# Kernel tuning notes

Measured on AMD Instinct MI355X. Metric: run time of the kernel, lower is better.

The kernel has to match this reference:

```python
import jax, jax.numpy as jnp
import numpy as np

EMBED = 128
NUM_HOPS = 3
VOCAB = 32000
MEM = 50
PAD = 0


def pos_weights(J, d):
    # MemN2N position encoding: 1 - (j+1)/J - (k+1)/d * (1 - 2*(j+1)/J)
    j = jnp.arange(J, dtype=jnp.float32)[:, None]
    k = jnp.arange(d, dtype=jnp.float32)[None, :]
    return 1.0 - (j + 1.0) / J - (k + 1.0) / d * (1.0 - 2.0 * (j + 1.0) / J)


def setup_inputs() -> dict:
    key = jax.random.key(0)
    ks = jax.random.split(key, 10)
    ctx_query = jax.random.randint(ks[0], (16, 10, 20), 0, VOCAB)
    story = jax.random.randint(ks[1], (16, MEM, 40), 0, VOCAB)

    def emb(k):
        w = 0.1 * jax.random.normal(k, (VOCAB, EMBED), dtype=jnp.float32)
        return w.at[PAD].set(0.0)  # padding_idx row is zero

    A_w = emb(ks[2])
    C_w = emb(ks[3])
    B_w = emb(ks[4])
    H_w = 0.1 * jax.random.normal(ks[5], (EMBED, EMBED), dtype=jnp.float32)
    H_b = 0.1 * jax.random.normal(ks[6], (EMBED,), dtype=jnp.float32)
    out_w = 0.1 * jax.random.normal(ks[7], (VOCAB, EMBED), dtype=jnp.float32)
    TA = 0.1 * jax.random.normal(ks[8], (MEM, EMBED), dtype=jnp.float32)
    TC = 0.1 * jax.random.normal(ks[9], (MEM, EMBED), dtype=jnp.float32)
    return {"ctx_query": ctx_query, "story": story, "A_w": A_w, "C_w": C_w,
            "B_w": B_w, "H_w": H_w, "H_b": H_b, "out_w": out_w, "TA": TA, "TC": TC}


def reference(ctx_query, story, A_w, C_w, B_w, H_w, H_b, out_w, TA, TC):
    B, NQ, S = ctx_query.shape
    R, S2 = story.shape[1], story.shape[2]
    cq = ctx_query.reshape(B * NQ, S)
    # story repeated across num_qa (broadcast instead of materialized repeat)
    st = jnp.broadcast_to(story[:, None], (B, NQ, R, S2)).reshape(B * NQ, R, S2)

    qw = pos_weights(S, EMBED)            # [S, d]
    state = jnp.sum(B_w[cq] * qw, axis=1)  # [BN, d]

    sw = pos_weights(S2, EMBED)           # [S2, d]
    for _ in range(NUM_HOPS):             # use_lw=True: A/C tied across hops
        mem = jnp.sum(A_w[st] * sw, axis=2) + TA    # [BN, R, d]
        outm = jnp.sum(C_w[st] * sw, axis=2) + TC   # [BN, R, d]
        probs = jax.nn.softmax(jnp.einsum('brd,bd->br', mem, state), axis=-1)
        response = jnp.einsum('br,brd->bd', probs, outm)  # [BN, d]
        state = response @ H_w.T + H_b + state      # H(response) + state
    return state @ out_w.T                          # [BN, vocab]
```

## Files before the change

kernel.cpp:

```cpp
#include <hip/hip_runtime.h>
#include <hip/hip_bf16.h>
#include <math.h>

#define EMBED 128
#define VOCAB 32000
#define MEMN  50
#define BATCH 16
#define NQ    10
#define SQ    20
#define SS    40
#define BN    (BATCH*NQ)
#define NHOPS 3

typedef short v8s __attribute__((ext_vector_type(8)));
typedef float v4f __attribute__((ext_vector_type(4)));

__device__ __forceinline__ float posw(int j, int J, int k) {
    float jf = (float)(j + 1) / (float)J;
    return 1.0f - jf - ((float)(k + 1) / (float)EMBED) * (1.0f - 2.0f * jf);
}

__device__ __forceinline__ short f2bf(float f) {
    __hip_bfloat16 h = __float2bfloat16(f);
    return *(short*)&h;
}

__global__ void k_embed(const int* __restrict__ cq, const int* __restrict__ story,
                        const float* __restrict__ Bw, const float* __restrict__ Aw,
                        const float* __restrict__ Cw, const float* __restrict__ TA,
                        const float* __restrict__ TC, const float* __restrict__ Hw,
                        float* __restrict__ state, float* __restrict__ memb,
                        float* __restrict__ outb, float* __restrict__ HwT) {
    int blk = blockIdx.x;
    int t = threadIdx.x;
    if (blk < BN) {
        float acc = 0.f;
        #pragma unroll
        for (int s = 0; s < SQ; ++s) {
            int tok = cq[blk * SQ + s];
            acc += Bw[tok * EMBED + t] * posw(s, SQ, t);
        }
        state[blk * EMBED + t] = acc;
    } else if (blk < BN + BATCH * MEMN) {
        int br = blk - BN;
        int r = br % MEMN;
        float ma = TA[r * EMBED + t];
        float mc = TC[r * EMBED + t];
        const int* toks = story + br * SS;
        #pragma unroll 4
        for (int s = 0; s < SS; ++s) {
            int tok = toks[s];
            float w = posw(s, SS, t);
            ma += Aw[tok * EMBED + t] * w;
            mc += Cw[tok * EMBED + t] * w;
        }
        memb[br * EMBED + t] = ma;
        outb[br * EMBED + t] = mc;
    } else {
        int k = blk - (BN + BATCH * MEMN);
        HwT[k * EMBED + t] = Hw[t * EMBED + k];
    }
}

__global__ void k_hops(const float* __restrict__ memb, const float* __restrict__ outb,
                       const float* __restrict__ HwT, const float* __restrict__ Hb,
                       const float* __restrict__ state, __hip_bfloat16* __restrict__ stateF) {
    __shared__ float lmem[MEMN][EMBED + 1];
    __shared__ float lout[MEMN][EMBED + 1];
    __shared__ float lstate[EMBED];
    __shared__ float lprobs[MEMN];
    __shared__ float lresp[EMBED];
    int bn = blockIdx.x;
    int b  = bn / NQ;
    int t  = threadIdx.x;
    for (int i = t; i < MEMN * EMBED; i += EMBED) {
        int r = i >> 7, d = i & 127;
        lmem[r][d] = memb[b * MEMN * EMBED + i];
        lout[r][d] = outb[b * MEMN * EMBED + i];
    }
    lstate[t] = state[bn * EMBED + t];
    __syncthreads();

    for (int hop = 0; hop < NHOPS; ++hop) {
        float logit = -1e30f;
        if (t < MEMN) {
            float acc = 0.f;
            for (int d = 0; d < EMBED; ++d) acc += lmem[t][d] * lstate[d];
            logit = acc;
        }
        if (t < 64) {
            float m = logit;
            #pragma unroll
            for (int off = 32; off; off >>= 1) m = fmaxf(m, __shfl_xor(m, off, 64));
            float e = (t < MEMN) ? __expf(logit - m) : 0.f;
            float ssum = e;
            #pragma unroll
            for (int off = 32; off; off >>= 1) ssum += __shfl_xor(ssum, off, 64);
            if (t < MEMN) lprobs[t] = e / ssum;
        }
        __syncthreads();
        float resp = 0.f;
        for (int r = 0; r < MEMN; ++r) resp += lprobs[r] * lout[r][t];
        lresp[t] = resp;
        __syncthreads();
        float acc = Hb[t] + lstate[t];
        for (int k = 0; k < EMBED; ++k) acc += lresp[k] * HwT[k * EMBED + t];
        __syncthreads();
        lstate[t] = acc;
        __syncthreads();
    }
    int frag = ((t >> 5) << 2) | ((t >> 3) & 3);
    stateF[((size_t)frag * BN + bn) * 8 + (t & 7)] = __float2bfloat16(lstate[t]);
}

__global__ __launch_bounds__(64) void k_out(const __hip_bfloat16* __restrict__ stateF,
                                            const float* __restrict__ outw,
                                            float* __restrict__ out) {
    int l = threadIdx.x;
    int col16 = l & 15;
    int kg = l >> 4;
    int vbase = blockIdx.x << 4;
    int v = vbase + col16;

    v8s bfrag[4];
    #pragma unroll
    for (int k4 = 0; k4 < 4; ++k4) {
        const float4* p = (const float4*)&outw[(size_t)v * EMBED + k4 * 32 + kg * 8];
        float4 w0 = p[0], w1 = p[1];
        v8s bf;
        bf[0] = f2bf(w0.x); bf[1] = f2bf(w0.y); bf[2] = f2bf(w0.z); bf[3] = f2bf(w0.w);
        bf[4] = f2bf(w1.x); bf[5] = f2bf(w1.y); bf[6] = f2bf(w1.z); bf[7] = f2bf(w1.w);
        bfrag[k4] = bf;
    }

    v4f acc[10];
    #pragma unroll
    for (int m = 0; m < 10; ++m) acc[m] = (v4f){0.f, 0.f, 0.f, 0.f};

    const v8s* aF = (const v8s*)stateF;
    #pragma unroll
    for (int k4 = 0; k4 < 4; ++k4) {
        v8s af[10];
        #pragma unroll
        for (int m = 0; m < 10; ++m)
            af[m] = aF[(((k4 << 2) | kg) * BN) + m * 16 + col16];
        #pragma unroll
        for (int m = 0; m < 10; ++m)
            acc[m] = __builtin_amdgcn_mfma_f32_16x16x32_bf16(af[m], bfrag[k4], acc[m], 0, 0, 0);
    }

    #pragma unroll
    for (int m = 0; m < 10; ++m) {
        #pragma unroll
        for (int i = 0; i < 4; ++i)
            out[(size_t)(m * 16 + kg * 4 + i) * VOCAB + v] = acc[m][i];
    }
}

extern "C" void kernel_launch(void* const* d_in, const int* in_sizes, int n_in,
                              void* d_out, int out_size, void* d_ws, size_t ws_size,
                              hipStream_t stream) {
    const int*   ctx_query = (const int*)  d_in[0];
    const int*   story     = (const int*)  d_in[1];
    const float* A_w       = (const float*)d_in[2];
    const float* C_w       = (const float*)d_in[3];
    const float* B_w       = (const float*)d_in[4];
    const float* H_w       = (const float*)d_in[5];
    const float* H_b       = (const float*)d_in[6];
    const float* out_w     = (const float*)d_in[7];
    const float* TA        = (const float*)d_in[8];
    const float* TC        = (const float*)d_in[9];
    float* out = (float*)d_out;

    float* ws    = (float*)d_ws;
    float* state = ws;
    float* memb  = state + BN * EMBED;
    float* outb  = memb + BATCH * MEMN * EMBED;
    float* HwT   = outb + BATCH * MEMN * EMBED;
    __hip_bfloat16* stateF = (__hip_bfloat16*)(HwT + EMBED * EMBED);

    k_embed<<<BN + BATCH * MEMN + EMBED, EMBED, 0, stream>>>(
        ctx_query, story, B_w, A_w, C_w, TA, TC, H_w, state, memb, outb, HwT);
    k_hops<<<BN, EMBED, 0, stream>>>(memb, outb, HwT, H_b, state, stateF);
    k_out<<<VOCAB / 16, 64, 0, stream>>>(stateF, out_w, out);
}
```

Measured before the change: 36.78 us.

## Pre-convert output weights to bf16 in embed kernel and split A/C gathers

The fp32-to-bf16 conversion of out_w moves out of the output GEMM kernel and into extra blocks of the embedding kernel. There it runs alongside the gathers, and k_out then reads half the bytes. The A and C story gathers are split into separate blocks to raise parallelism, with full unrolling. The cost is an extra full write and read of an 8 MB bf16 copy of out_w in the workspace. The out_w read still happens once, just earlier, so the gain depends on overlap with the latency-bound embed work.

New measurement: 35.87 us. -2.5%, faster.

```diff
diff --git a/kernel.cpp b/kernel.cpp
--- a/kernel.cpp
+++ b/kernel.cpp
@@ -12,6 +12,13 @@
 #define BN    (BATCH*NQ)
 #define NHOPS 3
 
+#define G_QRY   BN
+#define G_STA   (G_QRY + BATCH*MEMN)
+#define G_STC   (G_STA + BATCH*MEMN)
+#define G_HT    (G_STC + EMBED)
+#define CONVROWS 64
+#define G_CONV  (G_HT + VOCAB/CONVROWS)
+
 typedef short v8s __attribute__((ext_vector_type(8)));
 typedef float v4f __attribute__((ext_vector_type(4)));
 
@@ -29,36 +36,56 @@
                         const float* __restrict__ Bw, const float* __restrict__ Aw,
                         const float* __restrict__ Cw, const float* __restrict__ TA,
                         const float* __restrict__ TC, const float* __restrict__ Hw,
+                        const float* __restrict__ outw,
                         float* __restrict__ state, float* __restrict__ memb,
-                        float* __restrict__ outb, float* __restrict__ HwT) {
+                        float* __restrict__ outb, float* __restrict__ HwT,
+                        __hip_bfloat16* __restrict__ owb) {
     int blk = blockIdx.x;
     int t = threadIdx.x;
-    if (blk < BN) {
+    if (blk < G_QRY) {
         float acc = 0.f;
+        const int* toks = cq + blk * SQ;
         #pragma unroll
         for (int s = 0; s < SQ; ++s) {
-            int tok = cq[blk * SQ + s];
+            int tok = toks[s];
             acc += Bw[tok * EMBED + t] * posw(s, SQ, t);
         }
         state[blk * EMBED + t] = acc;
-    } else if (blk < BN + BATCH * MEMN) {
-        int br = blk - BN;
+    } else if (blk < G_STA) {
+        int br = blk - G_QRY;
         int r = br % MEMN;
         float ma = TA[r * EMBED + t];
+        const int* toks = story + br * SS;
+        #pragma unroll
+        for (int s = 0; s < SS; ++s) {
+            int tok = toks[s];
+            ma += Aw[tok * EMBED + t] * posw(s, SS, t);
+        }
+        memb[br * EMBED + t] = ma;
+    } else if (blk < G_STC) {
+        int br = blk - G_STA;
+        int r = br % MEMN;
         float mc = TC[r * EMBED + t];
         const int* toks = story + br * SS;
-        #pragma unroll 4
+        #pragma unroll
         for (int s = 0; s < SS; ++s) {
             int tok = toks[s];
-            float w = posw(s, SS, t);
-            ma += Aw[tok * EMBED + t] * w;
-            mc += Cw[tok * EMBED + t] * w;
-        }
-        memb[br * EMBED + t] = ma;
+            mc += Cw[tok * EMBED + t] * posw(s, SS, t);
+        }
         outb[br * EMBED + t] = mc;
+    } else if (blk < G_HT) {
+        int k = blk - G_STC;
+        HwT[k * EMBED + t] = Hw[t * EMBED + k];
     } else {
-        int k = blk - (BN + BATCH * MEMN);
-        HwT[k * EMBED + t] = Hw[t * EMBED + k];
+        int base = (blk - G_HT) * (CONVROWS * EMBED);
+        #pragma unroll
+        for (int i = 0; i < 16; ++i) {
+            int e = base + i * 512 + t * 4;
+            float4 w = *(const float4*)&outw[e];
+            short4 p;
+            p.x = f2bf(w.x); p.y = f2bf(w.y); p.z = f2bf(w.z); p.w = f2bf(w.w);
+            *(short4*)&owb[e] = p;
+        }
     }
 }
 
@@ -73,10 +100,11 @@
     int bn = blockIdx.x;
     int b  = bn / NQ;
     int t  = threadIdx.x;
-    for (int i = t; i < MEMN * EMBED; i += EMBED) {
-        int r = i >> 7, d = i & 127;
-        lmem[r][d] = memb[b * MEMN * EMBED + i];
-        lout[r][d] = outb[b * MEMN * EMBED + i];
+    #pragma unroll
+    for (int i = 0; i < MEMN; ++i) {
+        int e = i * EMBED + t;
+        lmem[i][t] = memb[b * MEMN * EMBED + e];
+        lout[i][t] = outb[b * MEMN * EMBED + e];
     }
     lstate[t] = state[bn * EMBED + t];
     __syncthreads();
@@ -114,7 +142,7 @@
 }
 
 __global__ __launch_bounds__(64) void k_out(const __hip_bfloat16* __restrict__ stateF,
-                                            const float* __restrict__ outw,
+                                            const __hip_bfloat16* __restrict__ owb,
                                             float* __restrict__ out) {
     int l = threadIdx.x;
     int col16 = l & 15;
@@ -122,16 +150,11 @@
     int vbase = blockIdx.x << 4;
     int v = vbase + col16;
 
+    const v8s* bp = (const v8s*)owb;
     v8s bfrag[4];
     #pragma unroll
-    for (int k4 = 0; k4 < 4; ++k4) {
-        const float4* p = (const float4*)&outw[(size_t)v * EMBED + k4 * 32 + kg * 8];
-        float4 w0 = p[0], w1 = p[1];
-        v8s bf;
-        bf[0] = f2bf(w0.x); bf[1] = f2bf(w0.y); bf[2] = f2bf(w0.z); bf[3] = f2bf(w0.w);
-        bf[4] = f2bf(w1.x); bf[5] = f2bf(w1.y); bf[6] = f2bf(w1.z); bf[7] = f2bf(w1.w);
-        bfrag[k4] = bf;
-    }
+    for (int k4 = 0; k4 < 4; ++k4)
+        bfrag[k4] = bp[(size_t)v * 16 + k4 * 4 + kg];
 
     v4f acc[10];
     #pragma unroll
@@ -178,9 +201,11 @@
     float* outb  = memb + BATCH * MEMN * EMBED;
     float* HwT   = outb + BATCH * MEMN * EMBED;
     __hip_bfloat16* stateF = (__hip_bfloat16*)(HwT + EMBED * EMBED);
-
-    k_embed<<<BN + BATCH * MEMN + EMBED, EMBED, 0, stream>>>(
-        ctx_query, story, B_w, A_w, C_w, TA, TC, H_w, state, memb, outb, HwT);
-    k_hops<<<BN, EMBED, 0, stream>>>(memb, outb, HwT, H_b, state, stateF);
-    k_out<<<VOCAB / 16, 64, 0, stream>>>(stateF, out_w, out);
-}
+    __hip_bfloat16* owb    = stateF + BN * EMBED;
+
+    k_embed<<<G_CONV, 128, 0, stream>>>(
+        ctx_query, story, B_w, A_w, C_w, TA, TC, H_w, out_w,
+        state, memb, outb, HwT, owb);
+    k_hops<<<BN, 128, 0, stream>>>(memb, outb, HwT, H_b, state, stateF);
+    k_out<<<VOCAB / 16, 64, 0, stream>>>(stateF, owb, out);
+}
```

## Fuse hops and output GEMM into one kernel with atomic-counter handoff

Applied to the files above, without the earlier changes.

Merges the hop kernel and the vocabulary projection into a single launch. 160 blocks run the hops while 250 GEMM blocks prefetch and convert their out_w tiles to bf16, then spin on a global counter until every hop block has published its state. The hop blocks now use 256 threads with split reductions and read H_w directly, which drops the transpose work from the embed kernel. This removes one launch and overlaps weight loading with the serial hop chain. The cost is a spin-wait that assumes all 410 blocks can be resident at once, plus a smaller number of GEMM blocks each handling two tiles.

After: 124.6 us. +238.7%, slower.

```diff
diff --git a/kernel.cpp b/kernel.cpp
--- a/kernel.cpp
+++ b/kernel.cpp
@@ -12,8 +12,14 @@
 #define BN    (BATCH*NQ)
 #define NHOPS 3
 
+#define NHOPSBLK 160
+#define NGEMMBLK 250
+#define K2BLOCKS (NHOPSBLK + NGEMMBLK)
+
 typedef short v8s __attribute__((ext_vector_type(8)));
 typedef float v4f __attribute__((ext_vector_type(4)));
+
+#define MFMA16 __builtin_amdgcn_mfma_f32_16x16x32_bf16
 
 __device__ __forceinline__ float posw(int j, int J, int k) {
     float jf = (float)(j + 1) / (float)J;
@@ -28,9 +34,9 @@
 __global__ void k_embed(const int* __restrict__ cq, const int* __restrict__ story,
                         const float* __restrict__ Bw, const float* __restrict__ Aw,
                         const float* __restrict__ Cw, const float* __restrict__ TA,
-                        const float* __restrict__ TC, const float* __restrict__ Hw,
+                        const float* __restrict__ TC,
                         float* __restrict__ state, float* __restrict__ memb,
-                        float* __restrict__ outb, float* __restrict__ HwT) {
+                        float* __restrict__ outb, unsigned* __restrict__ counter) {
     int blk = blockIdx.x;
     int t = threadIdx.x;
     if (blk < BN) {
@@ -57,103 +63,165 @@
         memb[br * EMBED + t] = ma;
         outb[br * EMBED + t] = mc;
     } else {
-        int k = blk - (BN + BATCH * MEMN);
-        HwT[k * EMBED + t] = Hw[t * EMBED + k];
+        if (t == 0) *counter = 0u;
     }
 }
 
-__global__ void k_hops(const float* __restrict__ memb, const float* __restrict__ outb,
-                       const float* __restrict__ HwT, const float* __restrict__ Hb,
-                       const float* __restrict__ state, __hip_bfloat16* __restrict__ stateF) {
+__global__ __launch_bounds__(256) void k_fused(const float* __restrict__ memb,
+                                               const float* __restrict__ outb,
+                                               const float* __restrict__ Hw,
+                                               const float* __restrict__ Hb,
+                                               const float* __restrict__ state,
+                                               const float* __restrict__ outw,
+                                               __hip_bfloat16* __restrict__ stateF,
+                                               unsigned* __restrict__ counter,
+                                               float* __restrict__ out) {
     __shared__ float lmem[MEMN][EMBED + 1];
     __shared__ float lout[MEMN][EMBED + 1];
     __shared__ float lstate[EMBED];
-    __shared__ float lprobs[MEMN];
-    __shared__ float lresp[EMBED];
-    int bn = blockIdx.x;
-    int b  = bn / NQ;
-    int t  = threadIdx.x;
-    for (int i = t; i < MEMN * EMBED; i += EMBED) {
-        int r = i >> 7, d = i & 127;
-        lmem[r][d] = memb[b * MEMN * EMBED + i];
-        lout[r][d] = outb[b * MEMN * EMBED + i];
-    }
-    lstate[t] = state[bn * EMBED + t];
-    __syncthreads();
-
-    for (int hop = 0; hop < NHOPS; ++hop) {
-        float logit = -1e30f;
-        if (t < MEMN) {
-            float acc = 0.f;
-            for (int d = 0; d < EMBED; ++d) acc += lmem[t][d] * lstate[d];
-            logit = acc;
-        }
-        if (t < 64) {
-            float m = logit;
-            #pragma unroll
-            for (int off = 32; off; off >>= 1) m = fmaxf(m, __shfl_xor(m, off, 64));
-            float e = (t < MEMN) ? __expf(logit - m) : 0.f;
-            float ssum = e;
-            #pragma unroll
-            for (int off = 32; off; off >>= 1) ssum += __shfl_xor(ssum, off, 64);
-            if (t < MEMN) lprobs[t] = e / ssum;
-        }
+    __shared__ float lpart[4][52];
+    __shared__ float lprobs[52];
+    __shared__ float lrespp[2][EMBED];
+    __shared__ float lHp[2][EMBED];
+
+    int blk = blockIdx.x;
+    int t = threadIdx.x;
+    int w = t >> 6;
+    int l = t & 63;
+
+    if (blk < NHOPSBLK) {
+        int bn = blk;
+        int b  = bn / NQ;
+        int d  = t & 127;
+        int h  = t >> 7;
+
+        {
+            const float4* mb4 = (const float4*)(memb + (size_t)b * MEMN * EMBED);
+            const float4* ob4 = (const float4*)(outb + (size_t)b * MEMN * EMBED);
+            for (int i = t; i < MEMN * EMBED / 4; i += 256) {
+                int r = i >> 5, c = (i & 31) << 2;
+                float4 v = mb4[i];
+                lmem[r][c] = v.x; lmem[r][c+1] = v.y; lmem[r][c+2] = v.z; lmem[r][c+3] = v.w;
+                float4 u = ob4[i];
+                lout[r][c] = u.x; lout[r][c+1] = u.y; lout[r][c+2] = u.z; lout[r][c+3] = u.w;
+            }
+            if (t < EMBED) lstate[t] = state[bn * EMBED + t];
+        }
+        float hbd = (t < EMBED) ? Hb[t] : 0.f;
         __syncthreads();
-        float resp = 0.f;
-        for (int r = 0; r < MEMN; ++r) resp += lprobs[r] * lout[r][t];
-        lresp[t] = resp;
+
+        for (int hop = 0; hop < NHOPS; ++hop) {
+            if (l < MEMN) {
+                int d0 = w << 5;
+                float a0 = 0.f, a1 = 0.f, a2 = 0.f, a3 = 0.f;
+                #pragma unroll
+                for (int j = 0; j < 32; j += 4) {
+                    a0 += lmem[l][d0 + j]     * lstate[d0 + j];
+                    a1 += lmem[l][d0 + j + 1] * lstate[d0 + j + 1];
+                    a2 += lmem[l][d0 + j + 2] * lstate[d0 + j + 2];
+                    a3 += lmem[l][d0 + j + 3] * lstate[d0 + j + 3];
+                }
+                lpart[w][l] = (a0 + a1) + (a2 + a3);
+            }
+            __syncthreads();
+            if (t < 64) {
+                float lg = (t < MEMN)
+                    ? (lpart[0][t] + lpart[1][t]) + (lpart[2][t] + lpart[3][t]) : -1e30f;
+                float mx = lg;
+                #pragma unroll
+                for (int off = 32; off; off >>= 1) mx = fmaxf(mx, __shfl_xor(mx, off, 64));
+                float e = (t < MEMN) ? __expf(lg - mx) : 0.f;
+                float ss = e;
+                #pragma unroll
+                for (int off = 32; off; off >>= 1) ss += __shfl_xor(ss, off, 64);
+                if (t < MEMN) lprobs[t] = e / ss;
+            }
+            __syncthreads();
+            {
+                float r0 = 0.f, r1 = 0.f;
+                int k0 = h * 25;
+                #pragma unroll
+                for (int k = 0; k < 24; k += 2) {
+                    r0 += lprobs[k0 + k]     * lout[k0 + k][d];
+                    r1 += lprobs[k0 + k + 1] * lout[k0 + k + 1][d];
+                }
+                r0 += lprobs[k0 + 24] * lout[k0 + 24][d];
+                lrespp[h][d] = r0 + r1;
+            }
+            __syncthreads();
+            {
+                int ks = h << 6;
+                const float4* hw4 = (const float4*)&Hw[(size_t)d * EMBED + ks];
+                float a0 = 0.f, a1 = 0.f, a2 = 0.f, a3 = 0.f;
+                #pragma unroll
+                for (int j = 0; j < 16; ++j) {
+                    float4 wv = hw4[j];
+                    int k = ks + (j << 2);
+                    a0 += (lrespp[0][k]     + lrespp[1][k])     * wv.x;
+                    a1 += (lrespp[0][k + 1] + lrespp[1][k + 1]) * wv.y;
+                    a2 += (lrespp[0][k + 2] + lrespp[1][k + 2]) * wv.z;
+                    a3 += (lrespp[0][k + 3] + lrespp[1][k + 3]) * wv.w;
+                }
+                lHp[h][d] = (a0 + a1) + (a2 + a3);
+            }
+            __syncthreads();
+            if (t < EMBED) {
+                float ns = hbd + lstate[t] + lHp[0][t] + lHp[1][t];
+                lstate[t] = ns;
+            }
+            __syncthreads();
+        }
+        if (t < EMBED) {
+            int frag = ((t >> 5) << 2) | ((t >> 3) & 3);
+            stateF[((size_t)frag * BN + bn) * 8 + (t & 7)] = __float2bfloat16(lstate[t]);
+        }
         __syncthreads();
-        float acc = Hb[t] + lstate[t];
-        for (int k = 0; k < EMBED; ++k) acc += lresp[k] * HwT[k * EMBED + t];
-        __syncthreads();
-        lstate[t] = acc;
-        __syncthreads();
-    }
-    int frag = ((t >> 5) << 2) | ((t >> 3) & 3);
-    stateF[((size_t)frag * BN + bn) * 8 + (t & 7)] = __float2bfloat16(lstate[t]);
-}
-
-__global__ __launch_bounds__(64) void k_out(const __hip_bfloat16* __restrict__ stateF,
-                                            const float* __restrict__ outw,
-                                            float* __restrict__ out) {
-    int l = threadIdx.x;
-    int col16 = l & 15;
-    int kg = l >> 4;
-    int vbase = blockIdx.x << 4;
-    int v = vbase + col16;
-
-    v8s bfrag[4];
-    #pragma unroll
-    for (int k4 = 0; k4 < 4; ++k4) {
-        const float4* p = (const float4*)&outw[(size_t)v * EMBED + k4 * 32 + kg * 8];
-        float4 w0 = p[0], w1 = p[1];
-        v8s bf;
-        bf[0] = f2bf(w0.x); bf[1] = f2bf(w0.y); bf[2] = f2bf(w0.z); bf[3] = f2bf(w0.w);
-        bf[4] = f2bf(w1.x); bf[5] = f2bf(w1.y); bf[6] = f2bf(w1.z); bf[7] = f2bf(w1.w);
-        bfrag[k4] = bf;
-    }
-
-    v4f acc[10];
-    #pragma unroll
-    for (int m = 0; m < 10; ++m) acc[m] = (v4f){0.f, 0.f, 0.f, 0.f};
-
-    const v8s* aF = (const v8s*)stateF;
-    #pragma unroll
-    for (int k4 = 0; k4 < 4; ++k4) {
-        v8s af[10];
+        if (t == 0)
+            __hip_atomic_fetch_add(counter, 1u, __ATOMIC_RELEASE, __HIP_MEMORY_SCOPE_AGENT);
+    } else {
+        int witem = (blk - NHOPSBLK) * 4 + w;
+        int col16 = l & 15;
+        int kg = l >> 4;
+        const v8s* aF = (const v8s*)stateF;
+
         #pragma unroll
-        for (int m = 0; m < 10; ++m)
-            af[m] = aF[(((k4 << 2) | kg) * BN) + m * 16 + col16];
-        #pragma unroll
-        for (int m = 0; m < 10; ++m)
-            acc[m] = __builtin_amdgcn_mfma_f32_16x16x32_bf16(af[m], bfrag[k4], acc[m], 0, 0, 0);
-    }
-
-    #pragma unroll
-    for (int m = 0; m < 10; ++m) {
-        #pragma unroll
-        for (int i = 0; i < 4; ++i)
-            out[(size_t)(m * 16 + kg * 4 + i) * VOCAB + v] = acc[m][i];
+        for (int it = 0; it < 2; ++it) {
+            int v = (witem + it * 1000) * 16 + col16;
+            v8s bfrag[4];
+            #pragma unroll
+            for (int k4 = 0; k4 < 4; ++k4) {
+                const float4* p = (const float4*)&outw[(size_t)v * EMBED + k4 * 32 + kg * 8];
+                float4 w0 = p[0], w1 = p[1];
+                v8s bf;
+                bf[0] = f2bf(w0.x); bf[1] = f2bf(w0.y); bf[2] = f2bf(w0.z); bf[3] = f2bf(w0.w);
+                bf[4] = f2bf(w1.x); bf[5] = f2bf(w1.y); bf[6] = f2bf(w1.z); bf[7] = f2bf(w1.w);
+                bfrag[k4] = bf;
+            }
+            if (it == 0) {
+                while (__hip_atomic_load(counter, __ATOMIC_ACQUIRE, __HIP_MEMORY_SCOPE_AGENT)
+                       < (unsigned)NHOPSBLK)
+                    __builtin_amdgcn_s_sleep(8);
+            }
+            v4f acc[10];
+            #pragma unroll
+            for (int m = 0; m < 10; ++m) acc[m] = (v4f){0.f, 0.f, 0.f, 0.f};
+            #pragma unroll
+            for (int k4 = 0; k4 < 4; ++k4) {
+                v8s af[10];
+                #pragma unroll
+                for (int m = 0; m < 10; ++m)
+                    af[m] = aF[(((k4 << 2) | kg) * BN) + m * 16 + col16];
+                #pragma unroll
+                for (int m = 0; m < 10; ++m)
+                    acc[m] = MFMA16(af[m], bfrag[k4], acc[m], 0, 0, 0);
+            }
+            #pragma unroll
+            for (int m = 0; m < 10; ++m) {
+                #pragma unroll
+                for (int i = 0; i < 4; ++i)
+                    out[(size_t)(m * 16 + kg * 4 + i) * VOCAB + v] = acc[m][i];
+            }
+        }
     }
 }
 
@@ -176,11 +244,11 @@
     float* state = ws;
     float* memb  = state + BN * EMBED;
     float* outb  = memb + BATCH * MEMN * EMBED;
-    float* HwT   = outb + BATCH * MEMN * EMBED;
-    __hip_bfloat16* stateF = (__hip_bfloat16*)(HwT + EMBED * EMBED);
-
-    k_embed<<<BN + BATCH * MEMN + EMBED, EMBED, 0, stream>>>(
-        ctx_query, story, B_w, A_w, C_w, TA, TC, H_w, state, memb, outb, HwT);
-    k_hops<<<BN, EMBED, 0, stream>>>(memb, outb, HwT, H_b, state, stateF);
-    k_out<<<VOCAB / 16, 64, 0, stream>>>(stateF, out_w, out);
-}
+    __hip_bfloat16* stateF = (__hip_bfloat16*)(outb + BATCH * MEMN * EMBED);
+    unsigned* counter = (unsigned*)(stateF + BN * EMBED);
+
+    k_embed<<<BN + BATCH * MEMN + 1, 128, 0, stream>>>(
+        ctx_query, story, B_w, A_w, C_w, TA, TC, state, memb, outb, counter);
+    k_fused<<<K2BLOCKS, 256, 0, stream>>>(
+        memb, outb, H_w, H_b, state, out_w, stateF, counter, out);
+}
```
